# Kernel tuning notes

Hardware: AMD Instinct MI355X
Metric: run time of the kernel (lower is better)

## Reference

```python
import jax, jax.numpy as jnp
import numpy as np

N_QUBITS = 6
N_LAYERS = 2
DIM = 2 ** N_QUBITS  # 64


def _apply_1q(state, U, q):
    """Apply a 1-qubit gate U on qubit q. state: (B, 2,...,2); U: (2,2) or (B,2,2)."""
    s = jnp.moveaxis(state, 1 + q, -1)
    if U.ndim == 3:  # batched gate (angle embedding)
        s = jnp.einsum('bij,b...j->b...i', U, s)
    else:
        s = jnp.einsum('ij,...j->...i', U, s)
    return jnp.moveaxis(s, -1, 1 + q)


def _cnot(state, c, t):
    """CNOT with control qubit c, target qubit t on (B, 2,...,2) state."""
    ax_c = 1 + c
    s0 = jax.lax.index_in_dim(state, 0, ax_c, keepdims=False)
    s1 = jax.lax.index_in_dim(state, 1, ax_c, keepdims=False)
    ax_t = 1 + t if t < c else t  # target axis index after removing control axis
    s1 = jnp.flip(s1, axis=ax_t)  # X on target where control=1
    return jnp.stack([s0, s1], axis=ax_c)


def _rot(phi, theta, omega):
    """PennyLane Rot(phi,theta,omega) = RZ(omega) RY(theta) RZ(phi), as a (2,2) complex matrix."""
    ct = jnp.cos(theta / 2)
    st = jnp.sin(theta / 2)
    ep = jnp.exp(-0.5j * (phi + omega))
    em = jnp.exp(0.5j * (phi - omega))
    row0 = jnp.stack([ep * ct, -em * st])
    row1 = jnp.stack([jnp.conj(em) * st, jnp.conj(ep) * ct])
    return jnp.stack([row0, row1]).astype(jnp.complex64)


def _circuit(angles, weights):
    """AngleEmbedding (RX) + StronglyEntanglingLayers + per-qubit <Z>. angles: (B, 6)."""
    B = angles.shape[0]
    state = jnp.zeros((B,) + (2,) * N_QUBITS, jnp.complex64)
    state = state.at[(slice(None),) + (0,) * N_QUBITS].set(1.0)

    # AngleEmbedding: RX(angle_q) on each qubit (batched gates)
    for q in range(N_QUBITS):
        half = angles[:, q] / 2
        ct = jnp.cos(half).astype(jnp.complex64)
        st = jnp.sin(half)
        U = jnp.stack([jnp.stack([ct, -1j * st], -1),
                       jnp.stack([-1j * st, ct], -1)], -2)  # (B,2,2)
        state = _apply_1q(state, U, q)

    # StronglyEntanglingLayers: per-layer Rot on each qubit, then CNOT ring with range r
    for l in range(N_LAYERS):
        for q in range(N_QUBITS):
            state = _apply_1q(state, _rot(weights[l, q, 0], weights[l, q, 1], weights[l, q, 2]), q)
        r = (l % (N_QUBITS - 1)) + 1
        for q in range(N_QUBITS):
            state = _cnot(state, q, (q + r) % N_QUBITS)

    probs = (state.real ** 2 + state.imag ** 2).reshape(B, DIM)  # (B, 64)
    # <Z_q> = sum_i probs[i] * (1 - 2*bit_q(i)); qubit 0 is the most-significant axis
    bits = (jnp.arange(DIM)[None, :] >> (N_QUBITS - 1 - jnp.arange(N_QUBITS))[:, None]) & 1
    signs = (1 - 2 * bits).astype(probs.dtype)  # (6, 64)
    return probs @ signs.T  # (B, 6)


def setup_inputs() -> dict:
    key = jax.random.key(0)
    k1, k2, k3, k4 = jax.random.split(key, 4)
    B, D = 65536, 512
    x = jax.random.normal(k1, (B, D), jnp.float32)
    W = jax.random.normal(k2, (N_QUBITS, D), jnp.float32) / np.float32(np.sqrt(D))
    b = jax.random.normal(k3, (N_QUBITS,), jnp.float32) * 0.01
    weights = jax.random.uniform(k4, (N_LAYERS, N_QUBITS, 3), jnp.float32, 0.0, 2 * np.pi)
    return {"x": x, "W": W, "b": b, "weights": weights}


def reference(x, W, b, weights):
    z = x @ W.T + b                                   # (B, 6)
    z = z / jnp.linalg.norm(z, axis=1, keepdims=True)  # L2 normalize per row
    return _circuit(z, weights)                        # (B, 6) Pauli-Z expvals
```

## Files before the change

kernel.cpp:

```cpp
#include <hip/hip_runtime.h>
#include <math.h>

#define NQ 6
#define NLAYERS 2
#define ROW_D 512

typedef short short8 __attribute__((ext_vector_type(8)));
typedef float f32x4 __attribute__((ext_vector_type(4)));

__device__ __forceinline__ ushort f2bf(float f) {
    unsigned u = __float_as_uint(f);
    return (ushort)((u + 0x7fffu + ((u >> 16) & 1u)) >> 16);
}

__device__ __forceinline__ float bcastf(float v, int srclane) {
    return __int_as_float(__builtin_amdgcn_readlane(__float_as_int(v), srclane));
}

__device__ __forceinline__ float merge_red(float u, float v, int m, int lane) {
    float send = (lane & m) ? u : v;
    float recv = __shfl_xor(send, m, 64);
    return ((lane & m) ? v : u) + recv;
}

__global__ __launch_bounds__(256) void gen_unitary(
    const float* __restrict__ weights, ushort* __restrict__ Mws)
{
    __shared__ __align__(16) float gmat[NLAYERS * NQ * 8];
    const int tid = threadIdx.x;
    if (tid < NLAYERS * NQ) {
        float phi = weights[tid * 3 + 0];
        float th  = weights[tid * 3 + 1];
        float om  = weights[tid * 3 + 2];
        float st, ct, sA, cA, sB, cB;
        __sincosf(0.5f * th, &st, &ct);
        __sincosf(0.5f * (phi + om), &sA, &cA);
        __sincosf(0.5f * (phi - om), &sB, &cB);
        float* g = &gmat[tid * 8];
        g[0] =  cA * ct;  g[1] = -sA * ct;
        g[2] = -cB * st;  g[3] = -sB * st;
        g[4] =  cA * ct;  g[5] =  sA * ct;
        g[6] =  cB * st;  g[7] = -sB * st;
    }
    __syncthreads();

    const int lane = tid & 63;
    const int wave = tid >> 6;
    const int jj = blockIdx.x * 4 + wave;

    int srcA = lane;
    #pragma unroll
    for (int q = NQ - 1; q >= 0; --q) {
        const int t = (q + 1) % NQ;
        srcA ^= ((srcA >> (5 - q)) & 1) << (5 - t);
    }
    int srcB = lane;
    #pragma unroll
    for (int q = NQ - 1; q >= 0; --q) {
        const int t = (q + 2) % NQ;
        srcB ^= ((srcB >> (5 - q)) & 1) << (5 - t);
    }
    const int adA = srcA << 2, adB = srcB << 2;

    float sr = (lane == jj) ? 1.f : 0.f;
    float si = 0.f;
    #pragma unroll
    for (int l = 0; l < NLAYERS; ++l) {
        #pragma unroll
        for (int q = 0; q < NQ; ++q) {
            const int bp = 5 - q, m = 1 << bp;
            const int bit = (lane >> bp) & 1;
            const float4 g = *reinterpret_cast<const float4*>(
                &gmat[((l * NQ + q) << 3) + (bit << 2)]);
            float pr = __shfl_xor(sr, m, 64);
            float pi = __shfl_xor(si, m, 64);
            float nr = g.x * sr - g.y * si + g.z * pr - g.w * pi;
            float ni = g.x * si + g.y * sr + g.z * pi + g.w * pr;
            sr = nr; si = ni;
        }
        const int ad = (l == 0) ? adA : adB;
        sr = __int_as_float(__builtin_amdgcn_ds_bpermute(ad, __float_as_int(sr)));
        si = __int_as_float(__builtin_amdgcn_ds_bpermute(ad, __float_as_int(si)));
    }

    const int pc = __popc(jj) & 3;
    float r2, i2;
    if      (pc == 1) { r2 =  si; i2 = -sr; }
    else if (pc == 2) { r2 = -sr; i2 = -si; }
    else if (pc == 3) { r2 = -si; i2 =  sr; }
    else              { r2 =  sr; i2 =  si; }
    Mws[lane * 64 + jj]        = f2bf(r2);
    Mws[4096 + lane * 64 + jj] = f2bf(i2);
}

__global__ __launch_bounds__(256) void qmain(
    const float* __restrict__ x, const float* __restrict__ W,
    const float* __restrict__ bvec, const ushort* __restrict__ Mws,
    float* __restrict__ out, int B)
{
    __shared__ short8 Mlds[2][64][8];
    __shared__ short8 wtile[4][16][8];
    const int tid = threadIdx.x;

    const short8* mg = reinterpret_cast<const short8*>(Mws);
    #pragma unroll
    for (int i = 0; i < 4; ++i) {
        const int idx = tid + i * 256;
        short8 v = mg[idx];
        const int mat = idx >> 9, row = (idx >> 3) & 63, c = idx & 7;
        Mlds[mat][row][c ^ (row & 7)] = v;
    }
    __syncthreads();

    const int lane = tid & 63;
    const int wave = tid >> 6;
    const int rowbase = blockIdx.x * 64 + wave * 16;

    float4 wv0[NQ], wv1[NQ];
    #pragma unroll
    for (int r = 0; r < NQ; ++r) {
        const float4* wr = reinterpret_cast<const float4*>(W + r * ROW_D);
        wv0[r] = wr[lane];
        wv1[r] = wr[lane + 64];
    }
    const int o = lane & 7;
    const int slot = (o < 6) ? o : (o - 2);
    const float bv = bvec[slot];

    ushort* wp = (ushort*)&wtile[wave][0][0];

    #pragma unroll 4
    for (int r16 = 0; r16 < 16; ++r16) {
        const float4* xr = reinterpret_cast<const float4*>(
            x + (size_t)(rowbase + r16) * ROW_D);
        const float4 xa = xr[lane];
        const float4 xb = xr[lane + 64];
        float p[NQ];
        #pragma unroll
        for (int r = 0; r < NQ; ++r) {
            p[r] = xa.x * wv0[r].x + xa.y * wv0[r].y + xa.z * wv0[r].z + xa.w * wv0[r].w
                 + xb.x * wv1[r].x + xb.y * wv1[r].y + xb.z * wv1[r].z + xb.w * wv1[r].w;
        }
        float A_ = merge_red(p[0], p[1], 1, lane);
        float Bm = merge_red(p[2], p[3], 1, lane);
        float C  = merge_red(p[4], p[5], 1, lane);
        float D_ = merge_red(A_, Bm, 2, lane);
        C += __shfl_xor(C, 2, 64);
        float E  = merge_red(D_, C, 4, lane);
        E += __shfl_xor(E, 8, 64);
        E += __shfl_xor(E, 16, 64);
        E += __shfl_xor(E, 32, 64);
        E += bv;

        float sq = (o < 6) ? E * E : 0.f;
        sq += __shfl_xor(sq, 1, 64);
        sq += __shfl_xor(sq, 2, 64);
        sq += __shfl_xor(sq, 4, 64);
        const float ang = 0.5f * E * rsqrtf(sq);
        float s_ang, c_ang;
        __sincosf(ang, &s_ang, &c_ang);

        float mag = 1.f;
        #pragma unroll
        for (int q = 0; q < NQ; ++q) {
            float cq  = bcastf(c_ang, q);
            float sq_ = bcastf(s_ang, q);
            mag *= ((lane >> (5 - q)) & 1) ? sq_ : cq;
        }
        wp[r16 * 64 + (((lane >> 3) ^ (r16 & 7)) << 3) + (lane & 7)] = f2bf(mag);
    }

    f32x4 cre[4] = {}, cim[4] = {};
    const int g4 = lane >> 4;
    const int lo3 = lane & 7;
    const short8 a0 = wtile[wave][lane & 15][(g4)     ^ lo3];
    const short8 a1 = wtile[wave][lane & 15][(4 + g4) ^ lo3];
    #pragma unroll
    for (int nt = 0; nt < 4; ++nt) {
        const int brow = nt * 16 + (lane & 15);
        const short8 br0 = Mlds[0][brow][(g4)     ^ lo3];
        const short8 br1 = Mlds[0][brow][(4 + g4) ^ lo3];
        const short8 bi0 = Mlds[1][brow][(g4)     ^ lo3];
        const short8 bi1 = Mlds[1][brow][(4 + g4) ^ lo3];
        cre[nt] = __builtin_amdgcn_mfma_f32_16x16x32_bf16(a0, br0, cre[nt], 0, 0, 0);
        cre[nt] = __builtin_amdgcn_mfma_f32_16x16x32_bf16(a1, br1, cre[nt], 0, 0, 0);
        cim[nt] = __builtin_amdgcn_mfma_f32_16x16x32_bf16(a0, bi0, cim[nt], 0, 0, 0);
        cim[nt] = __builtin_amdgcn_mfma_f32_16x16x32_bf16(a1, bi1, cim[nt], 0, 0, 0);
    }

    const int col = lane & 15;
    #pragma unroll
    for (int reg = 0; reg < 4; ++reg) {
        const float p0 = cre[0][reg] * cre[0][reg] + cim[0][reg] * cim[0][reg];
        const float p1 = cre[1][reg] * cre[1][reg] + cim[1][reg] * cim[1][reg];
        const float p2 = cre[2][reg] * cre[2][reg] + cim[2][reg] * cim[2][reg];
        const float p3 = cre[3][reg] * cre[3][reg] + cim[3][reg] * cim[3][reg];
        float t  = (p0 + p1) + (p2 + p3);
        float y0 = (p0 + p1) - (p2 + p3);
        float y1 = (p0 + p2) - (p1 + p3);
        #pragma unroll
        for (int m = 1; m <= 8; m <<= 1) {
            float rcv = __shfl_xor(t, m, 64);
            t = (lane & m) ? (rcv - t) : (t + rcv);
        }
        float y = merge_red(y0, y1, 1, lane);
        y += __shfl_xor(y, 2, 64);
        y += __shfl_xor(y, 4, 64);
        y += __shfl_xor(y, 8, 64);
        const size_t orow = (size_t)(rowbase + g4 * 4 + reg) * 6;
        if      (col == 0) { out[orow + 0] = y; }
        else if (col == 1) { out[orow + 1] = y; out[orow + 5] = t; }
        else if (col == 2) { out[orow + 4] = t; }
        else if (col == 4) { out[orow + 3] = t; }
        else if (col == 8) { out[orow + 2] = t; }
    }
}

extern "C" void kernel_launch(void* const* d_in, const int* in_sizes, int n_in,
                              void* d_out, int out_size, void* d_ws, size_t ws_size,
                              hipStream_t stream) {
    const float* x  = (const float*)d_in[0];
    const float* W  = (const float*)d_in[1];
    const float* bv = (const float*)d_in[2];
    const float* wt = (const float*)d_in[3];
    float* out = (float*)d_out;
    ushort* Mws = (ushort*)d_ws;
    const int B = in_sizes[0] / ROW_D;
    gen_unitary<<<16, 256, 0, stream>>>(wt, Mws);
    qmain<<<B / 64, 256, 0, stream>>>(x, W, bv, Mws, out, B);
}
```

Baseline: 38.39 us.

## Compute x@W^T projection with bf16 MFMA using hi/lo split of W

The projection z = x·W^T is moved from per-lane FMA dot products plus shuffle reductions onto 16x16x32 bf16 MFMA. W is split into bf16 hi and lo parts in the setup kernel, and the x tiles are converted to bf16 on the fly. The product-state amplitudes are then built directly in MFMA A-operand registers from per-row cos/sin values passed through LDS, so the per-row readlane loop disappears. This cuts VALU and shuffle work, at the cost of bf16 rounding of x (W keeps near-fp32 accuracy through the hi/lo split) and a larger LDS footprint.

New measurement: 37.57 us. -2.1%, faster.

```diff
diff --git a/kernel.cpp b/kernel.cpp
--- a/kernel.cpp
+++ b/kernel.cpp
@@ -12,22 +12,36 @@
     unsigned u = __float_as_uint(f);
     return (ushort)((u + 0x7fffu + ((u >> 16) & 1u)) >> 16);
 }
-
-__device__ __forceinline__ float bcastf(float v, int srclane) {
-    return __int_as_float(__builtin_amdgcn_readlane(__float_as_int(v), srclane));
-}
-
+__device__ __forceinline__ float bf2f(ushort h) {
+    return __uint_as_float((unsigned)h << 16);
+}
 __device__ __forceinline__ float merge_red(float u, float v, int m, int lane) {
     float send = (lane & m) ? u : v;
     float recv = __shfl_xor(send, m, 64);
     return ((lane & m) ? v : u) + recv;
 }
 
-__global__ __launch_bounds__(256) void gen_unitary(
-    const float* __restrict__ weights, ushort* __restrict__ Mws)
+__global__ __launch_bounds__(256) void gen_tables(
+    const float* __restrict__ weights, const float* __restrict__ W,
+    ushort* __restrict__ ws)
 {
+    const int tid = threadIdx.x;
+
+    {
+        const int base = (blockIdx.x * 256 + tid) * 2;
+        #pragma unroll
+        for (int e = 0; e < 2; ++e) {
+            const int i = base + e;
+            const int n = i >> 9;
+            const float v = (n < NQ) ? W[(n << 9) | (i & 511)] : 0.f;
+            const ushort hi = f2bf(v);
+            const ushort lo = f2bf(v - bf2f(hi));
+            ws[8192 + i]  = hi;
+            ws[16384 + i] = lo;
+        }
+    }
+
     __shared__ __align__(16) float gmat[NLAYERS * NQ * 8];
-    const int tid = threadIdx.x;
     if (tid < NLAYERS * NQ) {
         float phi = weights[tid * 3 + 0];
         float th  = weights[tid * 3 + 1];
@@ -89,20 +103,20 @@
     else if (pc == 2) { r2 = -sr; i2 = -si; }
     else if (pc == 3) { r2 = -si; i2 =  sr; }
     else              { r2 =  sr; i2 =  si; }
-    Mws[lane * 64 + jj]        = f2bf(r2);
-    Mws[4096 + lane * 64 + jj] = f2bf(i2);
+    ws[lane * 64 + jj]        = f2bf(r2);
+    ws[4096 + lane * 64 + jj] = f2bf(i2);
 }
 
 __global__ __launch_bounds__(256) void qmain(
-    const float* __restrict__ x, const float* __restrict__ W,
-    const float* __restrict__ bvec, const ushort* __restrict__ Mws,
-    float* __restrict__ out, int B)
+    const float* __restrict__ x, const float* __restrict__ bvec,
+    const ushort* __restrict__ ws, float* __restrict__ out, int B)
 {
     __shared__ short8 Mlds[2][64][8];
-    __shared__ short8 wtile[4][16][8];
+    __shared__ short8 Wlds[2][16][64];
+    __shared__ float2 trans[4][144];
     const int tid = threadIdx.x;
 
-    const short8* mg = reinterpret_cast<const short8*>(Mws);
+    const short8* mg = reinterpret_cast<const short8*>(ws);
     #pragma unroll
     for (int i = 0; i < 4; ++i) {
         const int idx = tid + i * 256;
@@ -110,85 +124,94 @@
         const int mat = idx >> 9, row = (idx >> 3) & 63, c = idx & 7;
         Mlds[mat][row][c ^ (row & 7)] = v;
     }
+    #pragma unroll
+    for (int i = 0; i < 8; ++i) {
+        const int idx = tid + i * 256;
+        short8 v = mg[1024 + idx];
+        const int mat = idx >> 10, n = (idx >> 6) & 15, c = idx & 63;
+        Wlds[mat][n][c ^ (n & 7)] = v;
+    }
     __syncthreads();
 
     const int lane = tid & 63;
     const int wave = tid >> 6;
+    const int g  = lane >> 4;
+    const int l4 = lane & 15;
+    const int swz = l4 & 7;
     const int rowbase = blockIdx.x * 64 + wave * 16;
 
-    float4 wv0[NQ], wv1[NQ];
-    #pragma unroll
-    for (int r = 0; r < NQ; ++r) {
-        const float4* wr = reinterpret_cast<const float4*>(W + r * ROW_D);
-        wv0[r] = wr[lane];
-        wv1[r] = wr[lane + 64];
-    }
-    const int o = lane & 7;
-    const int slot = (o < 6) ? o : (o - 2);
-    const float bv = bvec[slot];
-
-    ushort* wp = (ushort*)&wtile[wave][0][0];
-
+    f32x4 zacc = {0.f, 0.f, 0.f, 0.f};
+    const float* xrow = x + (size_t)(rowbase + l4) * ROW_D + g * 8;
     #pragma unroll 4
-    for (int r16 = 0; r16 < 16; ++r16) {
-        const float4* xr = reinterpret_cast<const float4*>(
-            x + (size_t)(rowbase + r16) * ROW_D);
-        const float4 xa = xr[lane];
-        const float4 xb = xr[lane + 64];
-        float p[NQ];
-        #pragma unroll
-        for (int r = 0; r < NQ; ++r) {
-            p[r] = xa.x * wv0[r].x + xa.y * wv0[r].y + xa.z * wv0[r].z + xa.w * wv0[r].w
-                 + xb.x * wv1[r].x + xb.y * wv1[r].y + xb.z * wv1[r].z + xb.w * wv1[r].w;
-        }
-        float A_ = merge_red(p[0], p[1], 1, lane);
-        float Bm = merge_red(p[2], p[3], 1, lane);
-        float C  = merge_red(p[4], p[5], 1, lane);
-        float D_ = merge_red(A_, Bm, 2, lane);
-        C += __shfl_xor(C, 2, 64);
-        float E  = merge_red(D_, C, 4, lane);
-        E += __shfl_xor(E, 8, 64);
-        E += __shfl_xor(E, 16, 64);
-        E += __shfl_xor(E, 32, 64);
-        E += bv;
-
-        float sq = (o < 6) ? E * E : 0.f;
-        sq += __shfl_xor(sq, 1, 64);
-        sq += __shfl_xor(sq, 2, 64);
-        sq += __shfl_xor(sq, 4, 64);
-        const float ang = 0.5f * E * rsqrtf(sq);
-        float s_ang, c_ang;
-        __sincosf(ang, &s_ang, &c_ang);
-
-        float mag = 1.f;
-        #pragma unroll
-        for (int q = 0; q < NQ; ++q) {
-            float cq  = bcastf(c_ang, q);
-            float sq_ = bcastf(s_ang, q);
-            mag *= ((lane >> (5 - q)) & 1) ? sq_ : cq;
-        }
-        wp[r16 * 64 + (((lane >> 3) ^ (r16 & 7)) << 3) + (lane & 7)] = f2bf(mag);
+    for (int kt = 0; kt < 16; ++kt) {
+        const float4 xa = *reinterpret_cast<const float4*>(xrow + kt * 32);
+        const float4 xb = *reinterpret_cast<const float4*>(xrow + kt * 32 + 4);
+        short8 af;
+        af[0] = (short)f2bf(xa.x); af[1] = (short)f2bf(xa.y);
+        af[2] = (short)f2bf(xa.z); af[3] = (short)f2bf(xa.w);
+        af[4] = (short)f2bf(xb.x); af[5] = (short)f2bf(xb.y);
+        af[6] = (short)f2bf(xb.z); af[7] = (short)f2bf(xb.w);
+        const int ch = (kt * 4 + g) ^ swz;
+        const short8 bh = Wlds[0][l4][ch];
+        const short8 bl = Wlds[1][l4][ch];
+        zacc = __builtin_amdgcn_mfma_f32_16x16x32_bf16(af, bh, zacc, 0, 0, 0);
+        zacc = __builtin_amdgcn_mfma_f32_16x16x32_bf16(af, bl, zacc, 0, 0, 0);
+    }
+
+    const float bn = (l4 < NQ) ? bvec[l4] : 0.f;
+    #pragma unroll
+    for (int reg = 0; reg < 4; ++reg) {
+        const float zv = zacc[reg] + bn;
+        float s2 = zv * zv;
+        s2 += __shfl_xor(s2, 1, 64);
+        s2 += __shfl_xor(s2, 2, 64);
+        s2 += __shfl_xor(s2, 4, 64);
+        s2 += __shfl_xor(s2, 8, 64);
+        const float ang = 0.5f * zv * rsqrtf(s2);
+        float sv, cv;
+        __sincosf(ang, &sv, &cv);
+        if (l4 < NQ)
+            trans[wave][(g * 4 + reg) * 9 + l4] = make_float2(cv, sv);
+    }
+
+    float cq[NQ], sq[NQ];
+    #pragma unroll
+    for (int q = 0; q < NQ; ++q) {
+        const float2 cs = trans[wave][l4 * 9 + q];
+        cq[q] = cs.x; sq[q] = cs.y;
+    }
+    float m45[4];
+    m45[0] = cq[4] * cq[5]; m45[1] = cq[4] * sq[5];
+    m45[2] = sq[4] * cq[5]; m45[3] = sq[4] * sq[5];
+    float pl[8];
+    #pragma unroll
+    for (int j = 0; j < 8; ++j)
+        pl[j] = ((j & 4) ? sq[3] : cq[3]) * m45[j & 3];
+    const float t12 = ((g & 2) ? sq[1] : cq[1]) * ((g & 1) ? sq[2] : cq[2]);
+    const float ph0 = cq[0] * t12;
+    const float ph1 = sq[0] * t12;
+    short8 a0, a1;
+    #pragma unroll
+    for (int j = 0; j < 8; ++j) {
+        a0[j] = (short)f2bf(ph0 * pl[j]);
+        a1[j] = (short)f2bf(ph1 * pl[j]);
     }
 
     f32x4 cre[4] = {}, cim[4] = {};
-    const int g4 = lane >> 4;
-    const int lo3 = lane & 7;
-    const short8 a0 = wtile[wave][lane & 15][(g4)     ^ lo3];
-    const short8 a1 = wtile[wave][lane & 15][(4 + g4) ^ lo3];
     #pragma unroll
     for (int nt = 0; nt < 4; ++nt) {
-        const int brow = nt * 16 + (lane & 15);
-        const short8 br0 = Mlds[0][brow][(g4)     ^ lo3];
-        const short8 br1 = Mlds[0][brow][(4 + g4) ^ lo3];
-        const short8 bi0 = Mlds[1][brow][(g4)     ^ lo3];
-        const short8 bi1 = Mlds[1][brow][(4 + g4) ^ lo3];
+        const int brow = nt * 16 + l4;
+        const short8 br0 = Mlds[0][brow][(g)     ^ swz];
+        const short8 br1 = Mlds[0][brow][(4 + g) ^ swz];
+        const short8 bi0 = Mlds[1][brow][(g)     ^ swz];
+        const short8 bi1 = Mlds[1][brow][(4 + g) ^ swz];
         cre[nt] = __builtin_amdgcn_mfma_f32_16x16x32_bf16(a0, br0, cre[nt], 0, 0, 0);
         cre[nt] = __builtin_amdgcn_mfma_f32_16x16x32_bf16(a1, br1, cre[nt], 0, 0, 0);
         cim[nt] = __builtin_amdgcn_mfma_f32_16x16x32_bf16(a0, bi0, cim[nt], 0, 0, 0);
         cim[nt] = __builtin_amdgcn_mfma_f32_16x16x32_bf16(a1, bi1, cim[nt], 0, 0, 0);
     }
 
-    const int col = lane & 15;
+    const int col = l4;
     #pragma unroll
     for (int reg = 0; reg < 4; ++reg) {
         const float p0 = cre[0][reg] * cre[0][reg] + cim[0][reg] * cim[0][reg];
@@ -207,7 +230,7 @@
         y += __shfl_xor(y, 2, 64);
         y += __shfl_xor(y, 4, 64);
         y += __shfl_xor(y, 8, 64);
-        const size_t orow = (size_t)(rowbase + g4 * 4 + reg) * 6;
+        const size_t orow = (size_t)(rowbase + g * 4 + reg) * 6;
         if      (col == 0) { out[orow + 0] = y; }
         else if (col == 1) { out[orow + 1] = y; out[orow + 5] = t; }
         else if (col == 2) { out[orow + 4] = t; }
@@ -224,8 +247,8 @@
     const float* bv = (const float*)d_in[2];
     const float* wt = (const float*)d_in[3];
     float* out = (float*)d_out;
-    ushort* Mws = (ushort*)d_ws;
+    ushort* ws = (ushort*)d_ws;
     const int B = in_sizes[0] / ROW_D;
-    gen_unitary<<<16, 256, 0, stream>>>(wt, Mws);
-    qmain<<<B / 64, 256, 0, stream>>>(x, W, bv, Mws, out, B);
-}
+    gen_tables<<<16, 256, 0, stream>>>(wt, W, ws);
+    qmain<<<B / 64, 256, 0, stream>>>(x, bv, ws, out, B);
+}
```
